# Kernel optimization log

Measured on AMD Instinct MI355X. Metric: run time of the kernel, lower is better.

## Reference

```python
import jax, jax.numpy as jnp
import numpy as np

B, S, D, F, A, H, O = 8, 2048, 64, 16, 32, 4, 64
HD = A // H  # head dim = 8
TWO_PI = 2.0 * np.pi


def setup_inputs() -> dict:
    key = jax.random.key(0)
    ks = jax.random.split(key, 10)
    sc = lambda k, sh, fan: (jax.random.normal(k, sh, jnp.float32) / np.sqrt(fan)).astype(jnp.float32)
    Din = D + 2 * D * F  # input width to gate/projection MLPs
    return dict(
        x=jax.random.normal(ks[0], (B, S, D), jnp.float32),
        freq_matrix=jnp.tile(jnp.linspace(1.0, 10.0, F, dtype=jnp.float32)[None, :], (D, 1)),
        phase=jax.random.normal(ks[1], (D, F), jnp.float32),
        freq_scale=jnp.ones((D, F), jnp.float32),
        Wq=sc(ks[2], (A, D), D), bq=jnp.zeros((A,), jnp.float32),          # query_proj
        Wk1=sc(ks[3], (A, 1), 1), bk1=jnp.zeros((A,), jnp.float32),        # key_proj (Linear(1, A))
        Wqi=sc(ks[4], (A, A), A), bqi=jnp.zeros((A,), jnp.float32),        # MHA in-proj (q slice)
        Wki=sc(ks[5], (A, A), A), bki=jnp.zeros((A,), jnp.float32),        # MHA in-proj (k slice)
        Wg=sc(ks[6], (O, Din), Din), bg=jnp.zeros((O,), jnp.float32),      # gate linear
        Wp=sc(ks[7], (O, Din), Din), bp=jnp.zeros((O,), jnp.float32),      # projection linear
    )


def reference(x, freq_matrix, phase, freq_scale, Wq, bq, Wk1, bk1, Wqi, bqi, Wki, bki, Wg, bg, Wp, bp):
    # x: [B, S, D]
    t = jnp.linspace(0.0, 1.0, S, dtype=x.dtype)                 # [S]
    f = freq_matrix * freq_scale                                 # [D, F]
    # fourier signal, batched over all input dims at once
    signal = TWO_PI * t[:, None, None] * f[None] + phase[None]   # [S, D, F]
    sin_f, cos_f = jnp.sin(signal), jnp.cos(signal)

    # MHA attention weights (averaged over heads) -- attn_out is discarded by the module
    queries = jnp.einsum('bsd,ad->bsa', x, Wq) + bq              # [B, S, A]
    q = (jnp.einsum('bsa,ea->bse', queries, Wqi) + bqi).reshape(B, S, H, HD)
    keys = f[:, :, None] * Wk1[None, None, :, 0] + bk1           # [D, F, A] via Linear(1, A)
    k = (jnp.einsum('dfa,ea->dfe', keys, Wki) + bki).reshape(D, F, H, HD)
    scores = jnp.einsum('bshe,dfhe->bdhsf', q, k) / np.sqrt(HD)  # [B, D, H, S, F]
    attn = jax.nn.softmax(scores, axis=-1).mean(axis=2)          # [B, D, S, F] (head-avg)
    aw = jnp.transpose(attn, (0, 2, 1, 3))                       # [B, S, D, F]

    # weighted fourier features; per-dim layout is [sin(F), cos(F)] to match torch cat order
    ff = jnp.concatenate([sin_f[None] * aw, cos_f[None] * aw], axis=-1)  # [B, S, D, 2F]
    ff = ff.reshape(B, S, D * 2 * F)

    ci = jnp.concatenate([x, ff], axis=-1)                       # [B, S, D + 2DF]
    gated = jax.nn.sigmoid(jnp.einsum('bsi,oi->bso', ci, Wg) + bg) * \
            jax.nn.silu(jnp.einsum('bsi,oi->bso', ci, Wp) + bp)
    return x + gated
```

## Files before the change

kernel.cpp:

```cpp
#include <hip/hip_runtime.h>
#include <math.h>

#define SS 2048
#define DIN 2112
#define NKT 66
#define TOK 16
#define NBLK 1024
#define ASTR 264
#define XSTR 68
#define XBSTR 72
#define CSTR 132
#define BFRAG_ELEMS (NKT * 8 * 64 * 8)
#define LOG2E 1.4426950408889634f
#define INV2PI 0.15915494309189535f

typedef __attribute__((ext_vector_type(4))) float f32x4;
typedef __attribute__((ext_vector_type(8))) short bf16x8;

__device__ __forceinline__ unsigned short f2bf(float x) {
    union { float f; unsigned u; } v; v.f = x;
    unsigned r = v.u + 0x7FFFu + ((v.u >> 16) & 1u);
    return (unsigned short)(r >> 16);
}

__device__ __forceinline__ unsigned pk2bf(float a, float b) {
    union { float f; unsigned u; } ua, ub; ua.f = a; ub.f = b;
    unsigned ra = ua.u + 0x7FFFu + ((ua.u >> 16) & 1u);
    unsigned rb = ub.u + 0x7FFFu + ((ub.u >> 16) & 1u);
#if __has_builtin(__builtin_amdgcn_perm)
    return __builtin_amdgcn_perm(rb, ra, 0x07060302u);
#else
    return (ra >> 16) | (rb & 0xFFFF0000u);
#endif
}

#if __has_builtin(__builtin_amdgcn_exp2f)
#define EXP2(x) __builtin_amdgcn_exp2f(x)
#else
#define EXP2(x) exp2f(x)
#endif
#if __has_builtin(__builtin_amdgcn_sinf)
#define SINR(x) __builtin_amdgcn_sinf(x)
#define COSR(x) __builtin_amdgcn_cosf(x)
#else
#define SINR(x) __sinf(6.283185307179586f * (x))
#define COSR(x) __cosf(6.283185307179586f * (x))
#endif

__global__ __launch_bounds__(256) void aff_pre(
    const float* __restrict__ Wq, const float* __restrict__ bq,
    const float* __restrict__ Wk1,
    const float* __restrict__ Wqi, const float* __restrict__ bqi,
    const float* __restrict__ Wki,
    const float* __restrict__ Wg, const float* __restrict__ Wp,
    float* __restrict__ ws)
{
    unsigned short* Bf = (unsigned short*)ws;
    float* WP = ws + 135168;
    float* cP = WP + 256;
    const int tid = threadIdx.x;
    const int gid = blockIdx.x * 256 + tid;

    {
        int j  = gid & 7;
        int q  = (gid >> 3) & 3;
        int nl = (gid >> 5) & 15;
        int nt = (gid >> 9) & 7;
        int kt = gid >> 12;
        int k = kt * 32 + q * 8 + j;
        int n = nt * 16 + nl;
        float s = (n < 64) ? Wg[(size_t)n * DIN + k] : Wp[(size_t)(n - 64) * DIN + k];
        int dst = ((kt * 8 + nt) * 64 + q * 16 + nl) * 8 + j;
        Bf[dst] = f2bf(s);
    }

    if (blockIdx.x == 0) {
        __shared__ float u[32];
        if (tid < 32) {
            float s = 0.f;
            #pragma unroll
            for (int a = 0; a < 32; ++a) s += Wki[tid * 32 + a] * Wk1[a];
            u[tid] = s;
        }
        __syncthreads();
        {
            const int h = tid >> 6;
            const int d = tid & 63;
            float s = 0.f;
            for (int j = 0; j < 8; ++j) {
                int e = h * 8 + j;
                float wc = 0.f;
                #pragma unroll
                for (int a = 0; a < 32; ++a) wc += Wqi[e * 32 + a] * Wq[a * 64 + d];
                s += u[e] * wc;
            }
            WP[h * 64 + d] = s * 0.35355339059327373f * LOG2E;
            if (d == 0) {
                float sc = 0.f;
                for (int j = 0; j < 8; ++j) {
                    int e = h * 8 + j;
                    float bcv = bqi[e];
                    #pragma unroll
                    for (int a = 0; a < 32; ++a) bcv += Wqi[e * 32 + a] * bq[a];
                    sc += u[e] * bcv;
                }
                cP[h] = sc * 0.35355339059327373f * LOG2E;
            }
        }
    }
}

__global__ __launch_bounds__(256, 4) void aff_main(
    const float* __restrict__ x,
    const float* __restrict__ fm, const float* __restrict__ fs,
    const float* __restrict__ phase,
    const unsigned short* __restrict__ Bf,
    const float* __restrict__ WP, const float* __restrict__ cP,
    const float* __restrict__ bg, const float* __restrict__ bp,
    float* __restrict__ out)
{
    __shared__ __align__(16) float xs[TOK * XSTR];
    __shared__ __align__(16) unsigned short xb[TOK * XBSTR];
    __shared__ __align__(16) unsigned short Ab[2][TOK * ASTR];
    __shared__ __align__(16) float fv[1024];
    __shared__ __align__(16) float phr[1024];
    __shared__ __align__(16) float Pl[TOK * 4];
    __shared__ __align__(16) float flmx[128];

    const int tid  = threadIdx.x;
    const int lane = tid & 63;
    const int w    = tid >> 6;
    const int t0   = blockIdx.x * TOK;
    const int lm   = lane & 15;
    const int lq   = lane >> 4;
    const int fh   = lq & 1;
    const int dsel = lane >> 5;
    const int dloc = (w << 1) + dsel;

    {
        float4 a = ((const float4*)fm)[tid];
        float4 b = ((const float4*)fs)[tid];
        float4 r; r.x = a.x * b.x; r.y = a.y * b.y; r.z = a.z * b.z; r.w = a.w * b.w;
        ((float4*)fv)[tid] = r;
        float4 p = ((const float4*)phase)[tid];
        p.x *= INV2PI; p.y *= INV2PI; p.z *= INV2PI; p.w *= INV2PI;
        ((float4*)phr)[tid] = p;
    }
    {
        int t = tid >> 4, j4 = (tid & 15) * 4;
        float4 xv = *(const float4*)(x + (size_t)(t0 + t) * 64 + j4);
        *(float4*)(xs + t * XSTR + j4) = xv;
        unsigned short* xbp = xb + t * XBSTR + j4;
        xbp[0] = f2bf(xv.x); xbp[1] = f2bf(xv.y); xbp[2] = f2bf(xv.z); xbp[3] = f2bf(xv.w);
    }
    __syncthreads();

    if (tid < 64) {
        int t = tid & 15, h = tid >> 4;
        float acc = cP[h];
        const float* wp = WP + h * 64;
        #pragma unroll 8
        for (int d = 0; d < 64; ++d) acc = fmaf(wp[d], xs[t * XSTR + d], acc);
        Pl[t * 4 + h] = acc;
    } else if (tid < 128) {
        int d = tid - 64;
        float mx = -1e30f, mn = 1e30f;
        #pragma unroll
        for (int f = 0; f < 16; ++f) {
            float v = fv[d * 16 + f];
            mx = fmaxf(mx, v); mn = fminf(mn, v);
        }
        flmx[d * 2] = mx; flmx[d * 2 + 1] = mn;
    }

    f32x4 acc0 = {}, acc1 = {};
    const bf16x8* Bv = (const bf16x8*)Bf;

    #pragma unroll
    for (int ks = 0; ks < 2; ++ks) {
        bf16x8 a = *(const bf16x8*)(xb + lm * XBSTR + ks * 32 + lq * 8);
        bf16x8 b0 = Bv[((size_t)ks * 8 + 2 * w) * 64 + lane];
        bf16x8 b1 = Bv[((size_t)ks * 8 + 2 * w + 1) * 64 + lane];
        acc0 = __builtin_amdgcn_mfma_f32_16x16x32_bf16(a, b0, acc0, 0, 0, 0);
        acc1 = __builtin_amdgcn_mfma_f32_16x16x32_bf16(a, b1, acc1, 0, 0, 0);
    }
    __syncthreads();

    const float w2 = (float)((t0 + lm) & (SS - 1)) * (1.0f / 2047.0f);

    auto build = [&](int ch, int buf) {
        const int d = ch * 8 + dloc;
        const float4 fA = *(const float4*)(fv + d * 16 + fh * 8);
        const float4 fB = *(const float4*)(fv + d * 16 + fh * 8 + 4);
        const float4 pA = *(const float4*)(phr + d * 16 + fh * 8);
        const float4 pB = *(const float4*)(phr + d * 16 + fh * 8 + 4);
        const float4 Pv = *(const float4*)(Pl + lm * 4);
        const float mxv = flmx[d * 2], mnv = flmx[d * 2 + 1];
        float fl[8] = {fA.x, fA.y, fA.z, fA.w, fB.x, fB.y, fB.z, fB.w};
        float pr[8] = {pA.x, pA.y, pA.z, pA.w, pB.x, pB.y, pB.z, pB.w};
        float aw[8] = {0.f, 0.f, 0.f, 0.f, 0.f, 0.f, 0.f, 0.f};
        float Ph4[4] = {Pv.x, Pv.y, Pv.z, Pv.w};
        #pragma unroll
        for (int h = 0; h < 4; ++h) {
            float Ph = Ph4[h];
            float m = fmaxf(mxv * Ph, mnv * Ph);
            float e[8]; float s = 0.f;
            #pragma unroll
            for (int j = 0; j < 8; ++j) { e[j] = EXP2(fmaf(fl[j], Ph, -m)); s += e[j]; }
            float z = s + __shfl_xor(s, 16);
            float inv = 0.25f / z;
            #pragma unroll
            for (int j = 0; j < 8; ++j) aw[j] = fmaf(e[j], inv, aw[j]);
        }
        unsigned sv[4], cv[4];
        #pragma unroll
        for (int jp = 0; jp < 4; ++jp) {
            int j0 = 2 * jp;
            float X0 = fmaf(w2, fl[j0], pr[j0]);
            float X1 = fmaf(w2, fl[j0 + 1], pr[j0 + 1]);
            float a0 = aw[j0], a1 = aw[j0 + 1];
            sv[jp] = pk2bf(a0 * SINR(X0), a1 * SINR(X1));
            cv[jp] = pk2bf(a0 * COSR(X0), a1 * COSR(X1));
        }
        unsigned short* dst = &Ab[buf][lm * ASTR + dloc * 32 + fh * 8];
        uint4 v0; v0.x = sv[0]; v0.y = sv[1]; v0.z = sv[2]; v0.w = sv[3];
        uint4 v1; v1.x = cv[0]; v1.y = cv[1]; v1.z = cv[2]; v1.w = cv[3];
        *(uint4*)dst = v0;
        *(uint4*)(dst + 16) = v1;
    };

    build(0, 0);
    __syncthreads();

    for (int ch = 0; ch < 8; ++ch) {
        const unsigned short* Ar = &Ab[ch & 1][0];
        #pragma unroll
        for (int ks = 0; ks < 8; ++ks) {
            const size_t kt = (size_t)(2 + ch * 8 + ks);
            bf16x8 a = *(const bf16x8*)(Ar + lm * ASTR + ks * 32 + lq * 8);
            bf16x8 b0 = Bv[(kt * 8 + 2 * w) * 64 + lane];
            bf16x8 b1 = Bv[(kt * 8 + 2 * w + 1) * 64 + lane];
            acc0 = __builtin_amdgcn_mfma_f32_16x16x32_bf16(a, b0, acc0, 0, 0, 0);
            acc1 = __builtin_amdgcn_mfma_f32_16x16x32_bf16(a, b1, acc1, 0, 0, 0);
        }
        if (ch < 7) build(ch + 1, (ch + 1) & 1);
        __syncthreads();
    }

    float* Cb = (float*)(&Ab[0][0]);
    #pragma unroll
    for (int r = 0; r < 4; ++r) {
        Cb[(lq * 4 + r) * CSTR + (2 * w) * 16 + lm]     = acc0[r];
        Cb[(lq * 4 + r) * CSTR + (2 * w + 1) * 16 + lm] = acc1[r];
    }
    __syncthreads();
    {
        int t = tid >> 4, o0 = (tid & 15) * 4;
        float4 g4 = *(float4*)(Cb + t * CSTR + o0);
        float4 p4 = *(float4*)(Cb + t * CSTR + 64 + o0);
        float4 bg4 = *(const float4*)(bg + o0);
        float4 bp4 = *(const float4*)(bp + o0);
        float4 xr = *(float4*)(xs + t * XSTR + o0);
        float4 o;
        { float g = g4.x + bg4.x, p = p4.x + bp4.x;
          o.x = fmaf(p * (1.f / (1.f + __expf(-g))), 1.f / (1.f + __expf(-p)), xr.x); }
        { float g = g4.y + bg4.y, p = p4.y + bp4.y;
          o.y = fmaf(p * (1.f / (1.f + __expf(-g))), 1.f / (1.f + __expf(-p)), xr.y); }
        { float g = g4.z + bg4.z, p = p4.z + bp4.z;
          o.z = fmaf(p * (1.f / (1.f + __expf(-g))), 1.f / (1.f + __expf(-p)), xr.z); }
        { float g = g4.w + bg4.w, p = p4.w + bp4.w;
          o.w = fmaf(p * (1.f / (1.f + __expf(-g))), 1.f / (1.f + __expf(-p)), xr.w); }
        *(float4*)(out + (size_t)(t0 + t) * 64 + o0) = o;
    }
}

extern "C" void kernel_launch(void* const* d_in, const int* in_sizes, int n_in,
                              void* d_out, int out_size, void* d_ws, size_t ws_size,
                              hipStream_t stream) {
    (void)in_sizes; (void)n_in; (void)out_size; (void)ws_size;
    const float* x    = (const float*)d_in[0];
    const float* fm   = (const float*)d_in[1];
    const float* phs  = (const float*)d_in[2];
    const float* fs   = (const float*)d_in[3];
    const float* Wq   = (const float*)d_in[4];
    const float* bq   = (const float*)d_in[5];
    const float* Wk1  = (const float*)d_in[6];
    const float* Wqi  = (const float*)d_in[8];
    const float* bqi  = (const float*)d_in[9];
    const float* Wki  = (const float*)d_in[10];
    const float* Wg   = (const float*)d_in[12];
    const float* bg   = (const float*)d_in[13];
    const float* Wp   = (const float*)d_in[14];
    const float* bp   = (const float*)d_in[15];
    float* out = (float*)d_out;
    float* ws  = (float*)d_ws;

    aff_pre<<<BFRAG_ELEMS / 256, 256, 0, stream>>>(Wq, bq, Wk1, Wqi, bqi, Wki, Wg, Wp, ws);

    const unsigned short* Bf = (const unsigned short*)ws;
    const float* WP = ws + 135168;
    const float* cP = WP + 256;
    aff_main<<<NBLK, 256, 0, stream>>>(x, fm, fs, phs, Bf, WP, cP, bg, bp, out);
}
```

Baseline: 120.1 us.

## Double tokens per block and share B fragments across two M-tiles

Each block now handles 32 tokens with 512 threads (8 waves). Each wave owns one 16-column N-tile and both 16-token M-tiles, so every bf16 weight fragment loaded from global memory feeds two MFMAs, halving weight traffic per token. The frequency, phase and min/max tables are computed once in the prep kernel and read from the global workspace instead of being rebuilt in LDS by every block. The separate bf16 copy of x is dropped; the fp32 x tile is converted on the fly. In exchange, register and LDS pressure per block rise, the grid halves, and build() now reads its tables from global/L2 rather than LDS.

```diff
diff --git a/kernel.cpp b/kernel.cpp
--- a/kernel.cpp
+++ b/kernel.cpp
@@ -4,16 +4,22 @@
 #define SS 2048
 #define DIN 2112
 #define NKT 66
-#define TOK 16
-#define NBLK 1024
+#define TOK 32
+#define NBLK 512
+#define NTHR 512
 #define ASTR 264
 #define XSTR 68
-#define XBSTR 72
 #define CSTR 132
 #define BFRAG_ELEMS (NKT * 8 * 64 * 8)
 #define LOG2E 1.4426950408889634f
 #define INV2PI 0.15915494309189535f
 
+#define OFF_WP 135168
+#define OFF_CP 135424
+#define OFF_FV 135680
+#define OFF_PH 136704
+#define OFF_MX 137728
+
 typedef __attribute__((ext_vector_type(4))) float f32x4;
 typedef __attribute__((ext_vector_type(8))) short bf16x8;
 
@@ -22,7 +28,6 @@
     unsigned r = v.u + 0x7FFFu + ((v.u >> 16) & 1u);
     return (unsigned short)(r >> 16);
 }
-
 __device__ __forceinline__ unsigned pk2bf(float a, float b) {
     union { float f; unsigned u; } ua, ub; ua.f = a; ub.f = b;
     unsigned ra = ua.u + 0x7FFFu + ((ua.u >> 16) & 1u);
@@ -53,11 +58,11 @@
     const float* __restrict__ Wqi, const float* __restrict__ bqi,
     const float* __restrict__ Wki,
     const float* __restrict__ Wg, const float* __restrict__ Wp,
+    const float* __restrict__ fm, const float* __restrict__ fs,
+    const float* __restrict__ phase,
     float* __restrict__ ws)
 {
     unsigned short* Bf = (unsigned short*)ws;
-    float* WP = ws + 135168;
-    float* cP = WP + 256;
     const int tid = threadIdx.x;
     const int gid = blockIdx.x * 256 + tid;
 
@@ -75,6 +80,31 @@
     }
 
     if (blockIdx.x == 0) {
+        float* WP = ws + OFF_WP;
+        float* cP = ws + OFF_CP;
+        float* fvg = ws + OFF_FV;
+        float* phg = ws + OFF_PH;
+        float* mxg = ws + OFF_MX;
+
+        {
+            float4 a = ((const float4*)fm)[tid];
+            float4 b = ((const float4*)fs)[tid];
+            float4 r; r.x = a.x * b.x; r.y = a.y * b.y; r.z = a.z * b.z; r.w = a.w * b.w;
+            ((float4*)fvg)[tid] = r;
+            float4 p = ((const float4*)phase)[tid];
+            p.x *= INV2PI; p.y *= INV2PI; p.z *= INV2PI; p.w *= INV2PI;
+            ((float4*)phg)[tid] = p;
+        }
+        if (tid < 64) {
+            float mx = -1e30f, mn = 1e30f;
+            #pragma unroll
+            for (int f = 0; f < 16; ++f) {
+                float v = fm[tid * 16 + f] * fs[tid * 16 + f];
+                mx = fmaxf(mx, v); mn = fminf(mn, v);
+            }
+            mxg[tid * 2] = mx; mxg[tid * 2 + 1] = mn;
+        }
+
         __shared__ float u[32];
         if (tid < 32) {
             float s = 0.f;
@@ -110,22 +140,23 @@
     }
 }
 
-__global__ __launch_bounds__(256, 4) void aff_main(
+__global__ __launch_bounds__(NTHR, 6) void aff_main(
     const float* __restrict__ x,
-    const float* __restrict__ fm, const float* __restrict__ fs,
-    const float* __restrict__ phase,
-    const unsigned short* __restrict__ Bf,
-    const float* __restrict__ WP, const float* __restrict__ cP,
+    const float* __restrict__ ws_c,
     const float* __restrict__ bg, const float* __restrict__ bp,
     float* __restrict__ out)
 {
     __shared__ __align__(16) float xs[TOK * XSTR];
-    __shared__ __align__(16) unsigned short xb[TOK * XBSTR];
     __shared__ __align__(16) unsigned short Ab[2][TOK * ASTR];
-    __shared__ __align__(16) float fv[1024];
-    __shared__ __align__(16) float phr[1024];
     __shared__ __align__(16) float Pl[TOK * 4];
-    __shared__ __align__(16) float flmx[128];
+
+    const unsigned short* Bfu = (const unsigned short*)ws_c;
+    const bf16x8* Bv = (const bf16x8*)Bfu;
+    const float* WP  = ws_c + OFF_WP;
+    const float* cP  = ws_c + OFF_CP;
+    const float* fvg = ws_c + OFF_FV;
+    const float* phg = ws_c + OFF_PH;
+    const float* mxg = ws_c + OFF_MX;
 
     const int tid  = threadIdx.x;
     const int lane = tid & 63;
@@ -135,67 +166,54 @@
     const int lq   = lane >> 4;
     const int fh   = lq & 1;
     const int dsel = lane >> 5;
-    const int dloc = (w << 1) + dsel;
-
-    {
-        float4 a = ((const float4*)fm)[tid];
-        float4 b = ((const float4*)fs)[tid];
-        float4 r; r.x = a.x * b.x; r.y = a.y * b.y; r.z = a.z * b.z; r.w = a.w * b.w;
-        ((float4*)fv)[tid] = r;
-        float4 p = ((const float4*)phase)[tid];
-        p.x *= INV2PI; p.y *= INV2PI; p.z *= INV2PI; p.w *= INV2PI;
-        ((float4*)phr)[tid] = p;
-    }
+    const int dloc = ((w & 3) << 1) + dsel;
+    const int tb   = ((w >> 2) << 4) + lm;
+
     {
         int t = tid >> 4, j4 = (tid & 15) * 4;
         float4 xv = *(const float4*)(x + (size_t)(t0 + t) * 64 + j4);
         *(float4*)(xs + t * XSTR + j4) = xv;
-        unsigned short* xbp = xb + t * XBSTR + j4;
-        xbp[0] = f2bf(xv.x); xbp[1] = f2bf(xv.y); xbp[2] = f2bf(xv.z); xbp[3] = f2bf(xv.w);
     }
     __syncthreads();
 
-    if (tid < 64) {
-        int t = tid & 15, h = tid >> 4;
+    if (tid < 128) {
+        int t = tid & 31, h = tid >> 5;
         float acc = cP[h];
         const float* wp = WP + h * 64;
         #pragma unroll 8
         for (int d = 0; d < 64; ++d) acc = fmaf(wp[d], xs[t * XSTR + d], acc);
         Pl[t * 4 + h] = acc;
-    } else if (tid < 128) {
-        int d = tid - 64;
-        float mx = -1e30f, mn = 1e30f;
-        #pragma unroll
-        for (int f = 0; f < 16; ++f) {
-            float v = fv[d * 16 + f];
-            mx = fmaxf(mx, v); mn = fminf(mn, v);
-        }
-        flmx[d * 2] = mx; flmx[d * 2 + 1] = mn;
     }
 
     f32x4 acc0 = {}, acc1 = {};
-    const bf16x8* Bv = (const bf16x8*)Bf;
 
     #pragma unroll
     for (int ks = 0; ks < 2; ++ks) {
-        bf16x8 a = *(const bf16x8*)(xb + lm * XBSTR + ks * 32 + lq * 8);
-        bf16x8 b0 = Bv[((size_t)ks * 8 + 2 * w) * 64 + lane];
-        bf16x8 b1 = Bv[((size_t)ks * 8 + 2 * w + 1) * 64 + lane];
-        acc0 = __builtin_amdgcn_mfma_f32_16x16x32_bf16(a, b0, acc0, 0, 0, 0);
-        acc1 = __builtin_amdgcn_mfma_f32_16x16x32_bf16(a, b1, acc1, 0, 0, 0);
+        bf16x8 b = Bv[((size_t)ks * 8 + w) * 64 + lane];
+        #pragma unroll
+        for (int mt = 0; mt < 2; ++mt) {
+            const float* xr = xs + (mt * 16 + lm) * XSTR + ks * 32 + lq * 8;
+            float4 fa = *(const float4*)xr;
+            float4 fb = *(const float4*)(xr + 4);
+            union { unsigned u[4]; bf16x8 v; } av;
+            av.u[0] = pk2bf(fa.x, fa.y); av.u[1] = pk2bf(fa.z, fa.w);
+            av.u[2] = pk2bf(fb.x, fb.y); av.u[3] = pk2bf(fb.z, fb.w);
+            if (mt == 0) acc0 = __builtin_amdgcn_mfma_f32_16x16x32_bf16(av.v, b, acc0, 0, 0, 0);
+            else         acc1 = __builtin_amdgcn_mfma_f32_16x16x32_bf16(av.v, b, acc1, 0, 0, 0);
+        }
     }
     __syncthreads();
 
-    const float w2 = (float)((t0 + lm) & (SS - 1)) * (1.0f / 2047.0f);
+    const float w2 = (float)((t0 + tb) & (SS - 1)) * (1.0f / 2047.0f);
 
     auto build = [&](int ch, int buf) {
         const int d = ch * 8 + dloc;
-        const float4 fA = *(const float4*)(fv + d * 16 + fh * 8);
-        const float4 fB = *(const float4*)(fv + d * 16 + fh * 8 + 4);
-        const float4 pA = *(const float4*)(phr + d * 16 + fh * 8);
-        const float4 pB = *(const float4*)(phr + d * 16 + fh * 8 + 4);
-        const float4 Pv = *(const float4*)(Pl + lm * 4);
-        const float mxv = flmx[d * 2], mnv = flmx[d * 2 + 1];
+        const float4 fA = *(const float4*)(fvg + d * 16 + fh * 8);
+        const float4 fB = *(const float4*)(fvg + d * 16 + fh * 8 + 4);
+        const float4 pA = *(const float4*)(phg + d * 16 + fh * 8);
+        const float4 pB = *(const float4*)(phg + d * 16 + fh * 8 + 4);
+        const float4 Pv = *(const float4*)(Pl + tb * 4);
+        const float mxv = mxg[d * 2], mnv = mxg[d * 2 + 1];
         float fl[8] = {fA.x, fA.y, fA.z, fA.w, fB.x, fB.y, fB.z, fB.w};
         float pr[8] = {pA.x, pA.y, pA.z, pA.w, pB.x, pB.y, pB.z, pB.w};
         float aw[8] = {0.f, 0.f, 0.f, 0.f, 0.f, 0.f, 0.f, 0.f};
@@ -222,7 +240,7 @@
             sv[jp] = pk2bf(a0 * SINR(X0), a1 * SINR(X1));
             cv[jp] = pk2bf(a0 * COSR(X0), a1 * COSR(X1));
         }
-        unsigned short* dst = &Ab[buf][lm * ASTR + dloc * 32 + fh * 8];
+        unsigned short* dst = &Ab[buf][tb * ASTR + dloc * 32 + fh * 8];
         uint4 v0; v0.x = sv[0]; v0.y = sv[1]; v0.z = sv[2]; v0.w = sv[3];
         uint4 v1; v1.x = cv[0]; v1.y = cv[1]; v1.z = cv[2]; v1.w = cv[3];
         *(uint4*)dst = v0;
@@ -237,11 +255,11 @@
         #pragma unroll
         for (int ks = 0; ks < 8; ++ks) {
             const size_t kt = (size_t)(2 + ch * 8 + ks);
-            bf16x8 a = *(const bf16x8*)(Ar + lm * ASTR + ks * 32 + lq * 8);
-            bf16x8 b0 = Bv[(kt * 8 + 2 * w) * 64 + lane];
-            bf16x8 b1 = Bv[(kt * 8 + 2 * w + 1) * 64 + lane];
-            acc0 = __builtin_amdgcn_mfma_f32_16x16x32_bf16(a, b0, acc0, 0, 0, 0);
-            acc1 = __builtin_amdgcn_mfma_f32_16x16x32_bf16(a, b1, acc1, 0, 0, 0);
+            bf16x8 b  = Bv[(kt * 8 + w) * 64 + lane];
+            bf16x8 a0 = *(const bf16x8*)(Ar + lm * ASTR + ks * 32 + lq * 8);
+            bf16x8 a1 = *(const bf16x8*)(Ar + (16 + lm) * ASTR + ks * 32 + lq * 8);
+            acc0 = __builtin_amdgcn_mfma_f32_16x16x32_bf16(a0, b, acc0, 0, 0, 0);
+            acc1 = __builtin_amdgcn_mfma_f32_16x16x32_bf16(a1, b, acc1, 0, 0, 0);
         }
         if (ch < 7) build(ch + 1, (ch + 1) & 1);
         __syncthreads();
@@ -250,8 +268,8 @@
     float* Cb = (float*)(&Ab[0][0]);
     #pragma unroll
     for (int r = 0; r < 4; ++r) {
-        Cb[(lq * 4 + r) * CSTR + (2 * w) * 16 + lm]     = acc0[r];
-        Cb[(lq * 4 + r) * CSTR + (2 * w + 1) * 16 + lm] = acc1[r];
+        Cb[(lq * 4 + r) * CSTR + w * 16 + lm]        = acc0[r];
+        Cb[(16 + lq * 4 + r) * CSTR + w * 16 + lm]   = acc1[r];
     }
     __syncthreads();
     {
@@ -295,10 +313,7 @@
     float* out = (float*)d_out;
     float* ws  = (float*)d_ws;
 
-    aff_pre<<<BFRAG_ELEMS / 256, 256, 0, stream>>>(Wq, bq, Wk1, Wqi, bqi, Wki, Wg, Wp, ws);
-
-    const unsigned short* Bf = (const unsigned short*)ws;
-    const float* WP = ws + 135168;
-    const float* cP = WP + 256;
-    aff_main<<<NBLK, 256, 0, stream>>>(x, fm, fs, phs, Bf, WP, cP, bg, bp, out);
-}
+    aff_pre<<<BFRAG_ELEMS / 256, 256, 0, stream>>>(Wq, bq, Wk1, Wqi, bqi, Wki, Wg, Wp,
+                                                   fm, fs, phs, ws);
+    aff_main<<<NBLK, NTHR, 0, stream>>>(x, (const float*)ws, bg, bp, out);
+}
```

Result: slower. 126.7 us (+5.5%).
